# Kernel tuning notes

Hardware: AMD Instinct MI355X
Metric: run time of the kernel (lower is better)

Reference implementation:

```python
import jax, jax.numpy as jnp
import numpy as np

D_MODEL = 1024
NUM_HEADS = 16
HEAD_DIM = D_MODEL // NUM_HEADS
N = 4096


def setup_inputs() -> dict:
    key = jax.random.key(0)
    k_x, k_wqkv, k_bqkv, k_wo, k_bo = jax.random.split(key, 5)
    s_in = 1.0 / np.sqrt(D_MODEL)
    return {
        "x": jax.random.normal(k_x, (N, D_MODEL), dtype=jnp.float32),
        "w_qkv": jax.random.uniform(k_wqkv, (D_MODEL, 3 * D_MODEL), jnp.float32, -s_in, s_in),
        "b_qkv": jax.random.uniform(k_bqkv, (3 * D_MODEL,), jnp.float32, -s_in, s_in),
        "w_out": jax.random.uniform(k_wo, (D_MODEL, D_MODEL), jnp.float32, -s_in, s_in),
        "b_out": jax.random.uniform(k_bo, (D_MODEL,), jnp.float32, -s_in, s_in),
    }


def reference(x, w_qkv, b_qkv, w_out, b_out) -> jnp.ndarray:
    n, d = x.shape
    scale = HEAD_DIM ** -0.5
    # fused QKV projection: [N, 3D] -> [3, H, N, hd]
    qkv = (x @ w_qkv + b_qkv).reshape(n, 3, NUM_HEADS, HEAD_DIM).transpose(1, 2, 0, 3)
    q, k, v = qkv[0], qkv[1], qkv[2]
    attn = jax.nn.softmax(jnp.einsum("hnd,hmd->hnm", q, k) * scale, axis=-1)
    out = jnp.einsum("hnm,hmd->hnd", attn, v)  # [H, N, hd]
    out = out.transpose(1, 0, 2).reshape(n, d)
    return out @ w_out + b_out
```

## Files before the change

### kernel.cpp

```cpp
#include <hip/hip_runtime.h>
#include <hip/hip_bf16.h>

using bf16_t = __bf16;
using bf16x4 = __attribute__((ext_vector_type(4))) __bf16;
using bf16x8 = __attribute__((ext_vector_type(8))) __bf16;
using f32x4  = __attribute__((ext_vector_type(4))) float;
using f32x16 = __attribute__((ext_vector_type(16))) float;
using u32x2  = __attribute__((ext_vector_type(2))) unsigned;

#define N_TOK 4096
#define DM    1024
#define NH    16
#define HD    64
#define D3    3072

#if __has_builtin(__builtin_amdgcn_exp2f)
#define EXP2(x) __builtin_amdgcn_exp2f(x)
#else
extern "C" float __ocml_native_exp2_f32(float);
#define EXP2(x) __ocml_native_exp2_f32(x)
#endif

__device__ __forceinline__ void gl_lds16(const void* g, void* l) {
  __builtin_amdgcn_global_load_lds((const __attribute__((address_space(1))) void*)g,
                                   (__attribute__((address_space(3))) void*)l, 16, 0, 0);
}

__device__ __forceinline__ unsigned pkbf(float a, float b) {
  unsigned short la = __builtin_bit_cast(unsigned short, (bf16_t)a);
  unsigned short lb = __builtin_bit_cast(unsigned short, (bf16_t)b);
  return (unsigned)la | ((unsigned)lb << 16);
}

__device__ __forceinline__ bf16x8 mk8(unsigned a, unsigned b, unsigned c, unsigned d) {
  union { unsigned u[4]; bf16x8 v; } t;
  t.u[0] = a; t.u[1] = b; t.u[2] = c; t.u[3] = d;
  return t.v;
}

__device__ __forceinline__ void softmax_blk(const f32x16& sv, bf16x8& apA, bf16x8& apB) {
  float pp[16];
  #pragma unroll
  for (int r = 0; r < 16; r++) pp[r] = EXP2(sv[r]);
  unsigned w00 = pkbf(pp[0], pp[1]),   w01 = pkbf(pp[2], pp[3]);
  unsigned w10 = pkbf(pp[4], pp[5]),   w11 = pkbf(pp[6], pp[7]);
  unsigned w20 = pkbf(pp[8], pp[9]),   w21 = pkbf(pp[10], pp[11]);
  unsigned w30 = pkbf(pp[12], pp[13]), w31 = pkbf(pp[14], pp[15]);
  u32x2 r00 = __builtin_amdgcn_permlane32_swap(w00, w10, false, false);
  u32x2 r01 = __builtin_amdgcn_permlane32_swap(w01, w11, false, false);
  u32x2 r10 = __builtin_amdgcn_permlane32_swap(w20, w30, false, false);
  u32x2 r11 = __builtin_amdgcn_permlane32_swap(w21, w31, false, false);
  apA = mk8(r00[0], r01[0], r00[1], r01[1]);
  apB = mk8(r10[0], r11[0], r10[1], r11[1]);
}

__global__ void k_cvt_x(const float* __restrict__ x, bf16_t* __restrict__ xb) {
  int i = (blockIdx.x * blockDim.x + threadIdx.x) * 8;
  float4 f0 = *(const float4*)(x + i);
  float4 f1 = *(const float4*)(x + i + 4);
  bf16x8 v;
  v[0] = (bf16_t)f0.x; v[1] = (bf16_t)f0.y; v[2] = (bf16_t)f0.z; v[3] = (bf16_t)f0.w;
  v[4] = (bf16_t)f1.x; v[5] = (bf16_t)f1.y; v[6] = (bf16_t)f1.z; v[7] = (bf16_t)f1.w;
  *(bf16x8*)(xb + i) = v;
}

__global__ void k_transpose_cvt(const float* __restrict__ in, bf16_t* __restrict__ outh,
                                int R, int C) {
  __shared__ float tile[64][65];
  int r0 = blockIdx.y * 64, c0 = blockIdx.x * 64;
  int t = threadIdx.x;
  #pragma unroll
  for (int i = 0; i < 16; i++) {
    int idx = i * 256 + t; int r = idx >> 6, c = idx & 63;
    tile[r][c] = in[(size_t)(r0 + r) * C + (c0 + c)];
  }
  __syncthreads();
  #pragma unroll
  for (int i = 0; i < 16; i++) {
    int idx = i * 256 + t; int c = idx >> 6, r = idx & 63;
    outh[(size_t)(c0 + c) * R + (r0 + r)] = (bf16_t)tile[r][c];
  }
}

__global__ __launch_bounds__(256) void k_gemm_qkv(
    const bf16_t* __restrict__ A, const bf16_t* __restrict__ Bt,
    const float* __restrict__ bias, bf16_t* __restrict__ qkv, bf16_t* __restrict__ vT) {
  __shared__ bf16_t As[128 * 32];
  __shared__ bf16_t Bs[128 * 32];
  const int tid = threadIdx.x, wid = tid >> 6, lane = tid & 63;
  const int bid = blockIdx.x;
  const int brow = bid & 31;
  const int bcol = bid >> 5;
  const int wr = wid >> 1, wc = wid & 1;
  const int lrow = lane & 15, lk = (lane >> 4) * 8;

  f32x4 acc[4][4] = {};

  const int c0 = wid * 64 + lane;
  const int c1 = 256 + wid * 64 + lane;
  const bf16_t* Ab = A + (size_t)(brow * 128) * DM;
  const bf16_t* Bb = Bt + (size_t)(bcol * 128) * DM;

  for (int k0 = 0; k0 < DM; k0 += 32) {
    gl_lds16(Ab + (size_t)(c0 >> 2) * DM + k0 + (c0 & 3) * 8, As + (wid * 64) * 8);
    gl_lds16(Ab + (size_t)(c1 >> 2) * DM + k0 + (c1 & 3) * 8, As + (256 + wid * 64) * 8);
    gl_lds16(Bb + (size_t)(c0 >> 2) * DM + k0 + (c0 & 3) * 8, Bs + (wid * 64) * 8);
    gl_lds16(Bb + (size_t)(c1 >> 2) * DM + k0 + (c1 & 3) * 8, Bs + (256 + wid * 64) * 8);
    __syncthreads();
    bf16x8 a[4], b[4];
    #pragma unroll
    for (int m = 0; m < 4; m++) a[m] = *(const bf16x8*)(As + (wr * 64 + m * 16 + lrow) * 32 + lk);
    #pragma unroll
    for (int n = 0; n < 4; n++) b[n] = *(const bf16x8*)(Bs + (wc * 64 + n * 16 + lrow) * 32 + lk);
    #pragma unroll
    for (int m = 0; m < 4; m++)
      #pragma unroll
      for (int n = 0; n < 4; n++)
        acc[m][n] = __builtin_amdgcn_mfma_f32_16x16x32_bf16(a[m], b[n], acc[m][n], 0, 0, 0);
    __syncthreads();
  }

  const int row0 = brow * 128 + wr * 64, col0 = bcol * 128 + wc * 64;
  #pragma unroll
  for (int n = 0; n < 4; n++) {
    int col = col0 + n * 16 + lrow;
    int which = col >> 10, rem = col & 1023;
    int h = rem >> 6, d = rem & 63;
    float bv = bias[col];
    float scl = (which == 0) ? 0.18033688011112042f : 1.0f;
    if (which == 2) {
      bf16_t* ob = vT + ((size_t)h * HD + d) * N_TOK;
      #pragma unroll
      for (int m = 0; m < 4; m++) {
        int tok0 = row0 + m * 16 + (lane >> 4) * 4;
        bf16x4 pk;
        #pragma unroll
        for (int i = 0; i < 4; i++) pk[i] = (bf16_t)(acc[m][n][i] + bv);
        *(bf16x4*)(ob + tok0) = pk;
      }
    } else {
      bf16_t* ob = qkv + (size_t)(which * NH + h) * N_TOK * HD + d;
      #pragma unroll
      for (int m = 0; m < 4; m++)
        #pragma unroll
        for (int i = 0; i < 4; i++) {
          int row = row0 + m * 16 + (lane >> 4) * 4 + i;
          ob[(size_t)row * HD] = (bf16_t)((acc[m][n][i] + bv) * scl);
        }
    }
  }
}

__global__ __launch_bounds__(256, 4) void k_attn(
    const bf16_t* __restrict__ qkv, const bf16_t* __restrict__ vT,
    float* __restrict__ opart, float* __restrict__ lpart, int kv_chunk) {
  __shared__ bf16_t Kss[2][64 * 64];
  __shared__ bf16_t Vts[2][64 * 64];
  const int tid = threadIdx.x, wid = tid >> 6, lane = tid & 63;
  const int qb = blockIdx.x, h = blockIdx.y, kvs = blockIdx.z;
  const bf16_t* Q  = qkv + (size_t)h * N_TOK * HD;
  const bf16_t* K  = qkv + (size_t)(NH + h) * N_TOK * HD;
  const bf16_t* Vt = vT + (size_t)h * HD * N_TOK;
  const int L31 = lane & 31, h5 = lane >> 5, r7 = L31 & 7;

  const int kv_lo = kvs * kv_chunk;
  const int kv_hi = kv_lo + kv_chunk;

  const int sr0 = tid >> 3;
  const int sc0 = (tid & 7) ^ (sr0 & 7);

#define STAGE(B, KV0) do {                                                                  \
    gl_lds16(K  + (size_t)((KV0) + sr0)      * HD + sc0 * 8, &Kss[B][wid * 512]);           \
    gl_lds16(K  + (size_t)((KV0) + 32 + sr0) * HD + sc0 * 8, &Kss[B][2048 + wid * 512]);    \
    gl_lds16(Vt + (size_t)sr0        * N_TOK + (KV0) + sc0 * 8, &Vts[B][wid * 512]);        \
    gl_lds16(Vt + (size_t)(32 + sr0) * N_TOK + (KV0) + sc0 * 8, &Vts[B][2048 + wid * 512]); \
  } while (0)

  bf16x8 aq[4];
  {
    int qrow = qb * 128 + wid * 32 + L31;
    #pragma unroll
    for (int dc = 0; dc < 4; dc++)
      aq[dc] = *(const bf16x8*)(Q + (size_t)qrow * HD + dc * 16 + h5 * 8);
  }
  f32x16 o0 = {}, o1 = {}, l_acc = {};
  f32x16 fz = {};
  asm volatile("" : "+v"(fz));
  bf16x8 ones8;
  #pragma unroll
  for (int j = 0; j < 8; j++) ones8[j] = (bf16_t)1.0f;

  STAGE(0, kv_lo);
  __syncthreads();

  int buf = 0;
  for (int kv0 = kv_lo; kv0 < kv_hi; kv0 += 64) {
    if (kv0 + 64 < kv_hi) STAGE(buf ^ 1, kv0 + 64);
    const bf16_t* kb = &Kss[buf][0] + L31 * 64;
    const bf16_t* vb = &Vts[buf][0] + L31 * 64;

    __builtin_amdgcn_s_setprio(1);
    bf16x8 kf0 = *(const bf16x8*)(kb + (((0 + h5) ^ r7) * 8));
    bf16x8 kf1 = *(const bf16x8*)(kb + 2048 + (((0 + h5) ^ r7) * 8));
    f32x16 s0 = __builtin_amdgcn_mfma_f32_32x32x16_bf16(kf0, aq[0], fz, 0, 0, 0);
    f32x16 s1 = __builtin_amdgcn_mfma_f32_32x32x16_bf16(kf1, aq[0], fz, 0, 0, 0);
    #pragma unroll
    for (int dc = 1; dc < 4; dc++) {
      kf0 = *(const bf16x8*)(kb + (((dc * 2 + h5) ^ r7) * 8));
      s0 = __builtin_amdgcn_mfma_f32_32x32x16_bf16(kf0, aq[dc], s0, 0, 0, 0);
      kf1 = *(const bf16x8*)(kb + 2048 + (((dc * 2 + h5) ^ r7) * 8));
      s1 = __builtin_amdgcn_mfma_f32_32x32x16_bf16(kf1, aq[dc], s1, 0, 0, 0);
    }
    __builtin_amdgcn_s_setprio(0);

    bf16x8 ap0, ap1, ap2, ap3;
    softmax_blk(s0, ap0, ap1);
    __builtin_amdgcn_s_setprio(1);
    {
      bf16x8 vf;
      vf = *(const bf16x8*)(vb + (((0 + h5) ^ r7) * 8));
      o0 = __builtin_amdgcn_mfma_f32_32x32x16_bf16(ap0, vf, o0, 0, 0, 0);
      vf = *(const bf16x8*)(vb + (((2 + h5) ^ r7) * 8));
      o0 = __builtin_amdgcn_mfma_f32_32x32x16_bf16(ap1, vf, o0, 0, 0, 0);
      vf = *(const bf16x8*)(vb + 2048 + (((0 + h5) ^ r7) * 8));
      o1 = __builtin_amdgcn_mfma_f32_32x32x16_bf16(ap0, vf, o1, 0, 0, 0);
      vf = *(const bf16x8*)(vb + 2048 + (((2 + h5) ^ r7) * 8));
      o1 = __builtin_amdgcn_mfma_f32_32x32x16_bf16(ap1, vf, o1, 0, 0, 0);
      l_acc = __builtin_amdgcn_mfma_f32_32x32x16_bf16(ap0, ones8, l_acc, 0, 0, 0);
      l_acc = __builtin_amdgcn_mfma_f32_32x32x16_bf16(ap1, ones8, l_acc, 0, 0, 0);
    }
    __builtin_amdgcn_s_setprio(0);
    softmax_blk(s1, ap2, ap3);
    __builtin_amdgcn_s_setprio(1);
    {
      bf16x8 vf;
      vf = *(const bf16x8*)(vb + (((4 + h5) ^ r7) * 8));
      o0 = __builtin_amdgcn_mfma_f32_32x32x16_bf16(ap2, vf, o0, 0, 0, 0);
      vf = *(const bf16x8*)(vb + (((6 + h5) ^ r7) * 8));
      o0 = __builtin_amdgcn_mfma_f32_32x32x16_bf16(ap3, vf, o0, 0, 0, 0);
      vf = *(const bf16x8*)(vb + 2048 + (((4 + h5) ^ r7) * 8));
      o1 = __builtin_amdgcn_mfma_f32_32x32x16_bf16(ap2, vf, o1, 0, 0, 0);
      vf = *(const bf16x8*)(vb + 2048 + (((6 + h5) ^ r7) * 8));
      o1 = __builtin_amdgcn_mfma_f32_32x32x16_bf16(ap3, vf, o1, 0, 0, 0);
      l_acc = __builtin_amdgcn_mfma_f32_32x32x16_bf16(ap2, ones8, l_acc, 0, 0, 0);
      l_acc = __builtin_amdgcn_mfma_f32_32x32x16_bf16(ap3, ones8, l_acc, 0, 0, 0);
    }
    __builtin_amdgcn_s_setprio(0);

    __syncthreads();
    buf ^= 1;
  }
#undef STAGE

  if (L31 == 0) {
    float* lp = lpart + ((size_t)kvs * NH + h) * N_TOK + qb * 128 + wid * 32;
    #pragma unroll
    for (int r = 0; r < 16; r++)
      lp[(r & 3) + 8 * (r >> 2) + 4 * h5] = l_acc[r];
  }

  float* op = opart + (size_t)kvs * N_TOK * DM;
  #pragma unroll
  for (int r = 0; r < 16; r++) {
    int q32 = (r & 3) + 8 * (r >> 2) + 4 * h5;
    size_t base = (size_t)(qb * 128 + wid * 32 + q32) * DM + h * HD + L31;
    op[base] = o0[r];
    op[base + 32] = o1[r];
  }
}

__global__ __launch_bounds__(256) void k_combine(
    const float* __restrict__ opart, const float* __restrict__ lpart,
    bf16_t* __restrict__ oattn, int nsplit) {
  const int row = blockIdx.x, tid = threadIdx.x;
  const int col = tid * 4;
  const int h = col >> 6;
  const size_t idx = (size_t)row * DM + col;
  float4 a = *(const float4*)(opart + idx);
  float lsum = lpart[(size_t)h * N_TOK + row];
  for (int p = 1; p < nsplit; p++) {
    float4 b = *(const float4*)(opart + (size_t)p * N_TOK * DM + idx);
    a.x += b.x; a.y += b.y; a.z += b.z; a.w += b.w;
    lsum += lpart[((size_t)p * NH + h) * N_TOK + row];
  }
  float rl = 1.0f / lsum;
  bf16x4 hv;
  hv[0] = (bf16_t)(a.x * rl); hv[1] = (bf16_t)(a.y * rl);
  hv[2] = (bf16_t)(a.z * rl); hv[3] = (bf16_t)(a.w * rl);
  *(bf16x4*)(oattn + idx) = hv;
}

__global__ __launch_bounds__(256) void k_gemm_out(
    const bf16_t* __restrict__ A, const bf16_t* __restrict__ Bt,
    const float* __restrict__ bias, float* __restrict__ out) {
  __shared__ bf16_t As[128 * 32];
  __shared__ bf16_t Bs[128 * 32];
  const int tid = threadIdx.x, wid = tid >> 6, lane = tid & 63;
  const int bid = blockIdx.x;
  const int brow = bid & 31;
  const int bcol = bid >> 5;
  const int wr = wid >> 1, wc = wid & 1;
  const int lrow = lane & 15, lk = (lane >> 4) * 8;

  f32x4 acc[4][4] = {};

  const int c0 = wid * 64 + lane;
  const int c1 = 256 + wid * 64 + lane;
  const bf16_t* Ab = A + (size_t)(brow * 128) * DM;
  const bf16_t* Bb = Bt + (size_t)(bcol * 128) * DM;

  for (int k0 = 0; k0 < DM; k0 += 32) {
    gl_lds16(Ab + (size_t)(c0 >> 2) * DM + k0 + (c0 & 3) * 8, As + (wid * 64) * 8);
    gl_lds16(Ab + (size_t)(c1 >> 2) * DM + k0 + (c1 & 3) * 8, As + (256 + wid * 64) * 8);
    gl_lds16(Bb + (size_t)(c0 >> 2) * DM + k0 + (c0 & 3) * 8, Bs + (wid * 64) * 8);
    gl_lds16(Bb + (size_t)(c1 >> 2) * DM + k0 + (c1 & 3) * 8, Bs + (256 + wid * 64) * 8);
    __syncthreads();
    bf16x8 a[4], b[4];
    #pragma unroll
    for (int m = 0; m < 4; m++) a[m] = *(const bf16x8*)(As + (wr * 64 + m * 16 + lrow) * 32 + lk);
    #pragma unroll
    for (int n = 0; n < 4; n++) b[n] = *(const bf16x8*)(Bs + (wc * 64 + n * 16 + lrow) * 32 + lk);
    #pragma unroll
    for (int m = 0; m < 4; m++)
      #pragma unroll
      for (int n = 0; n < 4; n++)
        acc[m][n] = __builtin_amdgcn_mfma_f32_16x16x32_bf16(a[m], b[n], acc[m][n], 0, 0, 0);
    __syncthreads();
  }

  const int row0 = brow * 128 + wr * 64, col0 = bcol * 128 + wc * 64;
  #pragma unroll
  for (int n = 0; n < 4; n++) {
    int col = col0 + n * 16 + lrow;
    float bv = bias[col];
    #pragma unroll
    for (int m = 0; m < 4; m++)
      #pragma unroll
      for (int i = 0; i < 4; i++) {
        int row = row0 + m * 16 + (lane >> 4) * 4 + i;
        out[(size_t)row * DM + col] = acc[m][n][i] + bv;
      }
  }
}

extern "C" void kernel_launch(void* const* d_in, const int* in_sizes, int n_in,
                              void* d_out, int out_size, void* d_ws, size_t ws_size,
                              hipStream_t stream) {
  const float* x     = (const float*)d_in[0];
  const float* w_qkv = (const float*)d_in[1];
  const float* b_qkv = (const float*)d_in[2];
  const float* w_out = (const float*)d_in[3];
  const float* b_out = (const float*)d_in[4];
  float* out = (float*)d_out;

  char* ws = (char*)d_ws;
  bf16_t* qkv     = (bf16_t*)(ws);
  bf16_t* x_bf    = (bf16_t*)(ws + 25165824);
  bf16_t* wqkv_t  = (bf16_t*)(ws + 33554432);
  bf16_t* wout_t  = (bf16_t*)(ws + 39845888);
  bf16_t* attn    = (bf16_t*)(ws + 41943040);
  float*  lpart   = (float*)(ws + 50331648);
  float*  opart   = (float*)(ws + 51380224);
  bf16_t* vT      = qkv + (size_t)2 * NH * N_TOK * HD;

  const size_t OPBASE = 51380224ull;
  const size_t PART = (size_t)N_TOK * DM * 4;
  int nsplit = 1;
  if (ws_size >= OPBASE + 4 * PART) nsplit = 4;
  else if (ws_size >= OPBASE + 2 * PART) nsplit = 2;

  k_cvt_x<<<2048, 256, 0, stream>>>(x, x_bf);
  k_transpose_cvt<<<dim3(48, 16), 256, 0, stream>>>(w_qkv, wqkv_t, DM, D3);
  k_transpose_cvt<<<dim3(16, 16), 256, 0, stream>>>(w_out, wout_t, DM, DM);
  k_gemm_qkv<<<768, 256, 0, stream>>>(x_bf, wqkv_t, b_qkv, qkv, vT);
  k_attn<<<dim3(32, 16, nsplit), 256, 0, stream>>>(qkv, vT, opart, lpart, N_TOK / nsplit);
  k_combine<<<4096, 256, 0, stream>>>(opart, lpart, attn, nsplit);
  k_gemm_out<<<256, 256, 0, stream>>>(attn, wout_t, b_out, out);
}
```

Measured before the change: 177.6 us.

## Store attention partials in bf16, cut KV split, remap blocks, shrink out-GEMM tile

Attention partial outputs are written and read as bf16 instead of fp32, halving the partial buffer traffic between the attention and combine kernels. The KV split is reduced from up to 4 to at most 2, and the attention grid is flattened with an XCD-aware block remap (gid&7) so blocks sharing a head land on the same chiplet cache. The output GEMM tile shrinks from 128x128 to 64x128 to launch 512 blocks and fill more CUs. Rounding unnormalized partials to bf16 adds precision loss, and the smaller split gives less parallelism per block.

```diff
diff --git a/kernel.cpp b/kernel.cpp
--- a/kernel.cpp
+++ b/kernel.cpp
@@ -153,11 +153,14 @@
 
 __global__ __launch_bounds__(256, 4) void k_attn(
     const bf16_t* __restrict__ qkv, const bf16_t* __restrict__ vT,
-    float* __restrict__ opart, float* __restrict__ lpart, int kv_chunk) {
+    bf16_t* __restrict__ opart, float* __restrict__ lpart, int kv_chunk) {
   __shared__ bf16_t Kss[2][64 * 64];
   __shared__ bf16_t Vts[2][64 * 64];
   const int tid = threadIdx.x, wid = tid >> 6, lane = tid & 63;
-  const int qb = blockIdx.x, h = blockIdx.y, kvs = blockIdx.z;
+  const int chunkx = gridDim.x >> 3;
+  const int gid = blockIdx.x;
+  const int wgid = (gid & 7) * chunkx + (gid >> 3);
+  const int qb = wgid & 31, h = (wgid >> 5) & 15, kvs = wgid >> 9;
   const bf16_t* Q  = qkv + (size_t)h * N_TOK * HD;
   const bf16_t* K  = qkv + (size_t)(NH + h) * N_TOK * HD;
   const bf16_t* Vt = vT + (size_t)h * HD * N_TOK;
@@ -259,82 +262,82 @@
       lp[(r & 3) + 8 * (r >> 2) + 4 * h5] = l_acc[r];
   }
 
-  float* op = opart + (size_t)kvs * N_TOK * DM;
+  bf16_t* op = opart + (size_t)kvs * N_TOK * DM;
   #pragma unroll
   for (int r = 0; r < 16; r++) {
     int q32 = (r & 3) + 8 * (r >> 2) + 4 * h5;
     size_t base = (size_t)(qb * 128 + wid * 32 + q32) * DM + h * HD + L31;
-    op[base] = o0[r];
-    op[base + 32] = o1[r];
+    op[base] = (bf16_t)o0[r];
+    op[base + 32] = (bf16_t)o1[r];
   }
 }
 
 __global__ __launch_bounds__(256) void k_combine(
-    const float* __restrict__ opart, const float* __restrict__ lpart,
+    const bf16_t* __restrict__ opart, const float* __restrict__ lpart,
     bf16_t* __restrict__ oattn, int nsplit) {
   const int row = blockIdx.x, tid = threadIdx.x;
   const int col = tid * 4;
   const int h = col >> 6;
   const size_t idx = (size_t)row * DM + col;
-  float4 a = *(const float4*)(opart + idx);
+  bf16x4 b0 = *(const bf16x4*)(opart + idx);
+  float a[4] = {(float)b0[0], (float)b0[1], (float)b0[2], (float)b0[3]};
   float lsum = lpart[(size_t)h * N_TOK + row];
   for (int p = 1; p < nsplit; p++) {
-    float4 b = *(const float4*)(opart + (size_t)p * N_TOK * DM + idx);
-    a.x += b.x; a.y += b.y; a.z += b.z; a.w += b.w;
+    bf16x4 bp = *(const bf16x4*)(opart + (size_t)p * N_TOK * DM + idx);
+    #pragma unroll
+    for (int j = 0; j < 4; j++) a[j] += (float)bp[j];
     lsum += lpart[((size_t)p * NH + h) * N_TOK + row];
   }
   float rl = 1.0f / lsum;
   bf16x4 hv;
-  hv[0] = (bf16_t)(a.x * rl); hv[1] = (bf16_t)(a.y * rl);
-  hv[2] = (bf16_t)(a.z * rl); hv[3] = (bf16_t)(a.w * rl);
+  #pragma unroll
+  for (int j = 0; j < 4; j++) hv[j] = (bf16_t)(a[j] * rl);
   *(bf16x4*)(oattn + idx) = hv;
 }
 
 __global__ __launch_bounds__(256) void k_gemm_out(
     const bf16_t* __restrict__ A, const bf16_t* __restrict__ Bt,
     const float* __restrict__ bias, float* __restrict__ out) {
-  __shared__ bf16_t As[128 * 32];
+  __shared__ bf16_t As[64 * 32];
   __shared__ bf16_t Bs[128 * 32];
   const int tid = threadIdx.x, wid = tid >> 6, lane = tid & 63;
   const int bid = blockIdx.x;
-  const int brow = bid & 31;
-  const int bcol = bid >> 5;
+  const int brow = bid & 63;
+  const int bcol = bid >> 6;
   const int wr = wid >> 1, wc = wid & 1;
   const int lrow = lane & 15, lk = (lane >> 4) * 8;
 
-  f32x4 acc[4][4] = {};
+  f32x4 acc[2][4] = {};
 
   const int c0 = wid * 64 + lane;
-  const int c1 = 256 + wid * 64 + lane;
-  const bf16_t* Ab = A + (size_t)(brow * 128) * DM;
+  const bf16_t* Ab = A + (size_t)(brow * 64) * DM;
   const bf16_t* Bb = Bt + (size_t)(bcol * 128) * DM;
 
   for (int k0 = 0; k0 < DM; k0 += 32) {
     gl_lds16(Ab + (size_t)(c0 >> 2) * DM + k0 + (c0 & 3) * 8, As + (wid * 64) * 8);
-    gl_lds16(Ab + (size_t)(c1 >> 2) * DM + k0 + (c1 & 3) * 8, As + (256 + wid * 64) * 8);
     gl_lds16(Bb + (size_t)(c0 >> 2) * DM + k0 + (c0 & 3) * 8, Bs + (wid * 64) * 8);
-    gl_lds16(Bb + (size_t)(c1 >> 2) * DM + k0 + (c1 & 3) * 8, Bs + (256 + wid * 64) * 8);
-    __syncthreads();
-    bf16x8 a[4], b[4];
-    #pragma unroll
-    for (int m = 0; m < 4; m++) a[m] = *(const bf16x8*)(As + (wr * 64 + m * 16 + lrow) * 32 + lk);
+    gl_lds16(Bb + (size_t)((c0 + 256) >> 2) * DM + k0 + (c0 & 3) * 8, Bs + (256 + wid * 64) * 8);
+    __syncthreads();
+    bf16x8 a[2], b[4];
+    #pragma unroll
+    for (int m = 0; m < 2; m++) a[m] = *(const bf16x8*)(As + (wr * 32 + m * 16 + lrow) * 32 + lk);
     #pragma unroll
     for (int n = 0; n < 4; n++) b[n] = *(const bf16x8*)(Bs + (wc * 64 + n * 16 + lrow) * 32 + lk);
     #pragma unroll
-    for (int m = 0; m < 4; m++)
+    for (int m = 0; m < 2; m++)
       #pragma unroll
       for (int n = 0; n < 4; n++)
         acc[m][n] = __builtin_amdgcn_mfma_f32_16x16x32_bf16(a[m], b[n], acc[m][n], 0, 0, 0);
     __syncthreads();
   }
 
-  const int row0 = brow * 128 + wr * 64, col0 = bcol * 128 + wc * 64;
+  const int row0 = brow * 64 + wr * 32, col0 = bcol * 128 + wc * 64;
   #pragma unroll
   for (int n = 0; n < 4; n++) {
     int col = col0 + n * 16 + lrow;
     float bv = bias[col];
     #pragma unroll
-    for (int m = 0; m < 4; m++)
+    for (int m = 0; m < 2; m++)
       #pragma unroll
       for (int i = 0; i < 4; i++) {
         int row = row0 + m * 16 + (lane >> 4) * 4 + i;
@@ -360,20 +363,18 @@
   bf16_t* wout_t  = (bf16_t*)(ws + 39845888);
   bf16_t* attn    = (bf16_t*)(ws + 41943040);
   float*  lpart   = (float*)(ws + 50331648);
-  float*  opart   = (float*)(ws + 51380224);
+  bf16_t* opart   = (bf16_t*)(ws + 51380224);
   bf16_t* vT      = qkv + (size_t)2 * NH * N_TOK * HD;
 
   const size_t OPBASE = 51380224ull;
-  const size_t PART = (size_t)N_TOK * DM * 4;
-  int nsplit = 1;
-  if (ws_size >= OPBASE + 4 * PART) nsplit = 4;
-  else if (ws_size >= OPBASE + 2 * PART) nsplit = 2;
+  const size_t PART = (size_t)N_TOK * DM * 2;
+  const int nsplit = (ws_size >= OPBASE + 2 * PART) ? 2 : 1;
 
   k_cvt_x<<<2048, 256, 0, stream>>>(x, x_bf);
   k_transpose_cvt<<<dim3(48, 16), 256, 0, stream>>>(w_qkv, wqkv_t, DM, D3);
   k_transpose_cvt<<<dim3(16, 16), 256, 0, stream>>>(w_out, wout_t, DM, DM);
   k_gemm_qkv<<<768, 256, 0, stream>>>(x_bf, wqkv_t, b_qkv, qkv, vT);
-  k_attn<<<dim3(32, 16, nsplit), 256, 0, stream>>>(qkv, vT, opart, lpart, N_TOK / nsplit);
+  k_attn<<<512 * nsplit, 256, 0, stream>>>(qkv, vT, opart, lpart, N_TOK / nsplit);
   k_combine<<<4096, 256, 0, stream>>>(opart, lpart, attn, nsplit);
-  k_gemm_out<<<256, 256, 0, stream>>>(attn, wout_t, b_out, out);
-}
+  k_gemm_out<<<512, 256, 0, stream>>>(attn, wout_t, b_out, out);
+}
```

Result: faster. 163.9 us (median of 2 runs) (-7.7%).
